# Performance work log

Hardware: AMD Instinct MI355X
Metric: run time of the kernel (lower is better)

The kernel has to match this reference:

```python
import jax, jax.numpy as jnp
import numpy as np

B, L, D, H = 4, 2048, 1024, 16
DH = D // H
EPS = 1e-6

def layer_norm(x, g, b):
    mu = jnp.mean(x, axis=-1, keepdims=True)
    var = jnp.mean(jnp.square(x - mu), axis=-1, keepdims=True)
    return (x - mu) * jax.lax.rsqrt(var + EPS) * g + b

def setup_inputs() -> dict:
    key = jax.random.key(0)
    ks = jax.random.split(key, 8)
    s = 0.02
    return {
        "x": jax.random.normal(ks[0], (B, L, D), jnp.float32),
        "mask": jnp.ones((B, L), jnp.int32),
        "Wq": jax.random.normal(ks[1], (D, D), jnp.float32) * s,
        "bq": jnp.zeros((D,), jnp.float32),
        "Wk": jax.random.normal(ks[2], (D, D), jnp.float32) * s,
        "bk": jnp.zeros((D,), jnp.float32),
        "Wv": jax.random.normal(ks[3], (D, D), jnp.float32) * s,
        "bv": jnp.zeros((D,), jnp.float32),
        "g1": jnp.ones((D,), jnp.float32),
        "b1": jnp.zeros((D,), jnp.float32),
        "g2": jnp.ones((D,), jnp.float32),
        "b2": jnp.zeros((D,), jnp.float32),
        "Wo1": jax.random.normal(ks[4], (D, D), jnp.float32) * s,
        "bo1": jnp.zeros((D,), jnp.float32),
        "Wo2": jax.random.normal(ks[5], (D, D), jnp.float32) * s,
        "bo2": jnp.zeros((D,), jnp.float32),
    }

def reference(x, mask, Wq, bq, Wk, bk, Wv, bv, g1, b1, g2, b2, Wo1, bo1, Wo2, bo2):
    h = layer_norm(x, g1, b1)                                  # [B,L,D]
    q = (h @ Wq + bq).reshape(B, L, H, DH)
    k = (h @ Wk + bk).reshape(B, L, H, DH)
    v = (h @ Wv + bv).reshape(B, L, H, DH)
    scores = jnp.einsum('bqhd,bkhd->bhqk', q, k) / jnp.sqrt(jnp.float32(DH))
    m = mask.astype(scores.dtype)[:, None, None, :]            # [B,1,1,L]
    scores = scores + (1.0 - m) * (-1e30)                      # mask_logits
    probs = jax.nn.softmax(scores, axis=-1)
    attn = jnp.einsum('bhqk,bkhd->bqhd', probs, v).reshape(B, L, D)
    residual = x + attn
    out = layer_norm(residual, g2, b2)
    out = jax.nn.gelu(out @ Wo1 + bo1, approximate=False)      # exact GELU (nn.GELU)
    out = out @ Wo2 + bo2 + residual
    return out
```

## Files before the change

### kernel.cpp

```cpp
#include <hip/hip_runtime.h>
#include <stdint.h>
#include <math.h>

typedef __bf16 bf16_t;
typedef __bf16 bf16x8 __attribute__((ext_vector_type(8)));
typedef __bf16 bf16x4 __attribute__((ext_vector_type(4)));
typedef short short4v __attribute__((ext_vector_type(4)));
typedef float f32x4 __attribute__((ext_vector_type(4)));

#define B_ 4
#define L_ 2048
#define D_ 1024
#define H_ 16
#define DH_ 64
#define M_ (B_ * L_)
#define LOG2E 1.4426950408889634f
#define QSCALE 0.18033688011112042f

__device__ __forceinline__ void gload16(const bf16_t* gsrc, bf16_t* ldst) {
    __builtin_amdgcn_global_load_lds(
        (__attribute__((address_space(1))) void*)(void*)(gsrc),
        (__attribute__((address_space(3))) void*)(ldst), 16, 0, 0);
}

__device__ __forceinline__ float gelu_exact(float v) {
    return 0.5f * v * (1.0f + erff(v * 0.70710678118654752f));
}

__device__ __forceinline__ float fast_exp2(float x) {
#if __has_builtin(__builtin_amdgcn_exp2f)
    return __builtin_amdgcn_exp2f(x);
#else
    return exp2f(x);
#endif
}

__device__ __forceinline__ f32x4 mfma16(bf16x4 a, bf16x4 b, f32x4 c) {
#if __has_builtin(__builtin_amdgcn_mfma_f32_16x16x16_bf16)
    return __builtin_amdgcn_mfma_f32_16x16x16_bf16(a, b, c, 0, 0, 0);
#else
    union U { bf16x4 h; short4v s; };
    U ua, ub; ua.h = a; ub.h = b;
    return __builtin_amdgcn_mfma_f32_16x16x16bf16_1k(ua.s, ub.s, c, 0, 0, 0);
#endif
}

__global__ __launch_bounds__(256) void transpose5(const float* __restrict__ W0, const float* __restrict__ W1,
                                                  const float* __restrict__ W2, const float* __restrict__ W3,
                                                  const float* __restrict__ W4,
                                                  bf16_t* __restrict__ T0, bf16_t* __restrict__ T1,
                                                  bf16_t* __restrict__ T2, bf16_t* __restrict__ T3,
                                                  bf16_t* __restrict__ T4) {
    const float* W; bf16_t* T;
    switch (blockIdx.z) {
        case 0: W = W0; T = T0; break;
        case 1: W = W1; T = T1; break;
        case 2: W = W2; T = T2; break;
        case 3: W = W3; T = T3; break;
        default: W = W4; T = T4; break;
    }
    __shared__ float tile[32][33];
    const int x = threadIdx.x, y0 = threadIdx.y;
    const int bx = blockIdx.x * 32, by = blockIdx.y * 32;
    for (int kk = 0; kk < 4; ++kk)
        tile[y0 + kk * 8][x] = W[(size_t)(by + y0 + kk * 8) * D_ + bx + x];
    __syncthreads();
    for (int kk = 0; kk < 4; ++kk)
        T[(size_t)(bx + y0 + kk * 8) * D_ + by + x] = (bf16_t)tile[x][y0 + kk * 8];
}

__global__ __launch_bounds__(256) void maskbias_kernel(const int* __restrict__ mask,
                                                       float* __restrict__ mb) {
    const int i = blockIdx.x * 256 + threadIdx.x;
    mb[i] = mask[i] ? 0.f : -1.0e30f;
}

__global__ __launch_bounds__(256) void ln1_kernel(const float* __restrict__ x,
                                                  const float* __restrict__ g,
                                                  const float* __restrict__ b,
                                                  bf16_t* __restrict__ h) {
    const int row = blockIdx.x, t = threadIdx.x;
    const float4 v = *(const float4*)(x + (size_t)row * D_ + t * 4);
    float s = v.x + v.y + v.z + v.w;
    float s2 = v.x * v.x + v.y * v.y + v.z * v.z + v.w * v.w;
    for (int m = 1; m < 64; m <<= 1) { s += __shfl_xor(s, m, 64); s2 += __shfl_xor(s2, m, 64); }
    __shared__ float red[2][4];
    if ((t & 63) == 0) { red[0][t >> 6] = s; red[1][t >> 6] = s2; }
    __syncthreads();
    s = red[0][0] + red[0][1] + red[0][2] + red[0][3];
    s2 = red[1][0] + red[1][1] + red[1][2] + red[1][3];
    const float mean = s * (1.f / 1024.f);
    const float var = s2 * (1.f / 1024.f) - mean * mean;
    const float rstd = rsqrtf(var + 1e-6f);
    const float4 gv = *(const float4*)(g + t * 4);
    const float4 bv = *(const float4*)(b + t * 4);
    union { bf16_t h4[4]; uint2 u; } o;
    o.h4[0] = (bf16_t)((v.x - mean) * rstd * gv.x + bv.x);
    o.h4[1] = (bf16_t)((v.y - mean) * rstd * gv.y + bv.y);
    o.h4[2] = (bf16_t)((v.z - mean) * rstd * gv.z + bv.z);
    o.h4[3] = (bf16_t)((v.w - mean) * rstd * gv.w + bv.w);
    *(uint2*)(h + (size_t)row * D_ + t * 4) = o.u;
}

__global__ __launch_bounds__(256) void add_ln2_kernel(const float* __restrict__ x,
                                                      const bf16_t* __restrict__ attnb,
                                                      const float* __restrict__ g,
                                                      const float* __restrict__ b,
                                                      bf16_t* __restrict__ residb,
                                                      bf16_t* __restrict__ h) {
    const int row = blockIdx.x, t = threadIdx.x;
    const float4 xv = *(const float4*)(x + (size_t)row * D_ + t * 4);
    union { uint2 u; bf16_t h4[4]; } ai;
    ai.u = *(const uint2*)(attnb + (size_t)row * D_ + t * 4);
    float4 v;
    v.x = xv.x + (float)ai.h4[0]; v.y = xv.y + (float)ai.h4[1];
    v.z = xv.z + (float)ai.h4[2]; v.w = xv.w + (float)ai.h4[3];
    union { bf16_t h4[4]; uint2 u; } rs;
    rs.h4[0] = (bf16_t)v.x; rs.h4[1] = (bf16_t)v.y; rs.h4[2] = (bf16_t)v.z; rs.h4[3] = (bf16_t)v.w;
    *(uint2*)(residb + (size_t)row * D_ + t * 4) = rs.u;
    float s = v.x + v.y + v.z + v.w;
    float s2 = v.x * v.x + v.y * v.y + v.z * v.z + v.w * v.w;
    for (int m = 1; m < 64; m <<= 1) { s += __shfl_xor(s, m, 64); s2 += __shfl_xor(s2, m, 64); }
    __shared__ float red[2][4];
    if ((t & 63) == 0) { red[0][t >> 6] = s; red[1][t >> 6] = s2; }
    __syncthreads();
    s = red[0][0] + red[0][1] + red[0][2] + red[0][3];
    s2 = red[1][0] + red[1][1] + red[1][2] + red[1][3];
    const float mean = s * (1.f / 1024.f);
    const float var = s2 * (1.f / 1024.f) - mean * mean;
    const float rstd = rsqrtf(var + 1e-6f);
    const float4 gv = *(const float4*)(g + t * 4);
    const float4 bv = *(const float4*)(b + t * 4);
    union { bf16_t h4[4]; uint2 u; } o;
    o.h4[0] = (bf16_t)((v.x - mean) * rstd * gv.x + bv.x);
    o.h4[1] = (bf16_t)((v.y - mean) * rstd * gv.y + bv.y);
    o.h4[2] = (bf16_t)((v.z - mean) * rstd * gv.z + bv.z);
    o.h4[3] = (bf16_t)((v.w - mean) * rstd * gv.w + bv.w);
    *(uint2*)(h + (size_t)row * D_ + t * 4) = o.u;
}

__global__ __launch_bounds__(256) void gemm_qkv(const bf16_t* __restrict__ A,
                                                const bf16_t* __restrict__ BT,
                                                const float* __restrict__ bq,
                                                const float* __restrict__ bk,
                                                const float* __restrict__ bv,
                                                bf16_t* __restrict__ qb,
                                                bf16_t* __restrict__ kb,
                                                bf16_t* __restrict__ vb) {
    constexpr int K = 1024;
    __shared__ bf16_t As[128 * 32];
    __shared__ bf16_t Bs[128 * 32];
    const int t = threadIdx.x;
    const int wave = t >> 6, lane = t & 63;
    const int l16 = lane & 15, g4 = lane >> 4;
    const int bm = blockIdx.x * 128, bn = blockIdx.y * 128;
    const int wm = (wave >> 1) * 64, wn = (wave & 1) * 64;

    f32x4 acc[4][4];
    for (int i = 0; i < 4; ++i)
        for (int j = 0; j < 4; ++j) acc[i][j] = (f32x4){0.f, 0.f, 0.f, 0.f};

    const int ar = t >> 2, ak = (t & 3) * 8;
    const bf16_t* Ag = A + (size_t)(bm + ar) * K + ak;
    const bf16_t* Bg = BT + (size_t)(bn + ar) * K + ak;
    bf16_t* Al = As + t * 8;
    bf16_t* Bl = Bs + t * 8;

    for (int kk = 0; kk < K; kk += 32) {
        __syncthreads();
        gload16(Ag + kk, Al);
        gload16(Ag + (size_t)64 * K + kk, Al + 2048);
        gload16(Bg + kk, Bl);
        gload16(Bg + (size_t)64 * K + kk, Bl + 2048);
        __syncthreads();
        bf16x8 af[4], bfr[4];
        for (int i = 0; i < 4; ++i)
            af[i] = *(const bf16x8*)&As[(wm + i * 16 + l16) * 32 + g4 * 8];
        for (int j = 0; j < 4; ++j)
            bfr[j] = *(const bf16x8*)&Bs[(wn + j * 16 + l16) * 32 + g4 * 8];
        for (int i = 0; i < 4; ++i)
            for (int j = 0; j < 4; ++j)
                acc[i][j] = __builtin_amdgcn_mfma_f32_16x16x32_bf16(af[i], bfr[j], acc[i][j], 0, 0, 0);
    }

    const int which = bn >> 10;
    const int c0 = bn & 1023;
    const float* bias = (which == 0) ? bq : (which == 1) ? bk : bv;
    bf16_t* ob = (which == 0) ? qb : (which == 1) ? kb : vb;
    const float scale = (which == 0) ? QSCALE : 1.0f;

    for (int i = 0; i < 4; ++i)
        for (int j = 0; j < 4; ++j) {
            const int col = c0 + wn + j * 16 + l16;
            const float bvv = bias[col];
            const int row0 = bm + wm + i * 16 + g4 * 4;
            for (int r = 0; r < 4; ++r) {
                const float vv = (acc[i][j][r] + bvv) * scale;
                ob[(size_t)(row0 + r) * D_ + col] = (bf16_t)vv;
            }
        }
}

template <int MODE>
__global__ __launch_bounds__(256) void gemm_bt(const bf16_t* __restrict__ A,
                                               const bf16_t* __restrict__ BT,
                                               const float* __restrict__ bias,
                                               const bf16_t* __restrict__ residb,
                                               bf16_t* __restrict__ outb,
                                               float* __restrict__ outf) {
    constexpr int K = 1024, N = 1024;
    __shared__ bf16_t As[128 * 32];
    __shared__ bf16_t Bs[128 * 32];
    const int t = threadIdx.x;
    const int wave = t >> 6, lane = t & 63;
    const int l16 = lane & 15, g4 = lane >> 4;
    const int bm = blockIdx.x * 128, bn = blockIdx.y * 128;
    const int wm = (wave >> 1) * 64, wn = (wave & 1) * 64;

    f32x4 acc[4][4];
    for (int i = 0; i < 4; ++i)
        for (int j = 0; j < 4; ++j) acc[i][j] = (f32x4){0.f, 0.f, 0.f, 0.f};

    const int ar = t >> 2, ak = (t & 3) * 8;
    const bf16_t* Ag = A + (size_t)(bm + ar) * K + ak;
    const bf16_t* Bg = BT + (size_t)(bn + ar) * K + ak;
    bf16_t* Al = As + t * 8;
    bf16_t* Bl = Bs + t * 8;

    for (int kk = 0; kk < K; kk += 32) {
        __syncthreads();
        gload16(Ag + kk, Al);
        gload16(Ag + (size_t)64 * K + kk, Al + 2048);
        gload16(Bg + kk, Bl);
        gload16(Bg + (size_t)64 * K + kk, Bl + 2048);
        __syncthreads();
        bf16x8 af[4], bfr[4];
        for (int i = 0; i < 4; ++i)
            af[i] = *(const bf16x8*)&As[(wm + i * 16 + l16) * 32 + g4 * 8];
        for (int j = 0; j < 4; ++j)
            bfr[j] = *(const bf16x8*)&Bs[(wn + j * 16 + l16) * 32 + g4 * 8];
        for (int i = 0; i < 4; ++i)
            for (int j = 0; j < 4; ++j)
                acc[i][j] = __builtin_amdgcn_mfma_f32_16x16x32_bf16(af[i], bfr[j], acc[i][j], 0, 0, 0);
    }

    for (int i = 0; i < 4; ++i)
        for (int j = 0; j < 4; ++j) {
            const int col = bn + wn + j * 16 + l16;
            const float bv = bias[col];
            const int row0 = bm + wm + i * 16 + g4 * 4;
            for (int r = 0; r < 4; ++r) {
                float vv = acc[i][j][r] + bv;
                const size_t idx = (size_t)(row0 + r) * N + col;
                if (MODE == 1) {
                    outb[idx] = (bf16_t)gelu_exact(vv);
                } else {
                    outf[idx] = vv + (float)residb[idx];
                }
            }
        }
}

#define KS_STRIDE 72
#define VT_STRIDE 152
__global__ __launch_bounds__(256, 3) void attn_kernel(const bf16_t* __restrict__ q,
                                                      const bf16_t* __restrict__ k,
                                                      const bf16_t* __restrict__ v,
                                                      const float* __restrict__ maskbias,
                                                      bf16_t* __restrict__ attnb) {
    __shared__ char smem[18432 + 19456];
    bf16_t* Ks = (bf16_t*)smem;
    bf16_t* VT = (bf16_t*)(smem + 18432);
    bf16_t* Os = (bf16_t*)smem;

    const int t = threadIdx.x;
    const int wave = t >> 6, lane = t & 63;
    const int l16 = lane & 15, g4 = lane >> 4;
    const int id = blockIdx.x;
    const int xcd = id & 7, seq = id >> 3;
    const int bh = xcd * 8 + (seq >> 4);
    const int b = bh >> 4, h = bh & 15;
    const int q0 = (seq & 15) * 128;

    bf16x8 qf[2][2];
    for (int ti = 0; ti < 2; ++ti)
        for (int c = 0; c < 2; ++c)
            qf[ti][c] = *(const bf16x8*)(q + (size_t)(b * L_ + q0 + wave * 32 + ti * 16 + l16) * D_ +
                                         h * DH_ + c * 32 + g4 * 8);

    f32x4 accO[2][5];
    for (int ti = 0; ti < 2; ++ti)
        for (int dt = 0; dt < 5; ++dt) accO[ti][dt] = (f32x4){0.f, 0.f, 0.f, 0.f};

    const bf16_t one_or_zero = (l16 == 0) ? (bf16_t)1.0f : (bf16_t)0.0f;
    const bf16x4 ones4 = (bf16x4){one_or_zero, one_or_zero, one_or_zero, one_or_zero};

    for (int k0 = 0; k0 < L_; k0 += 128) {
        __syncthreads();
        for (int cc = 0; cc < 4; ++cc) {
            const int c = t + cc * 256;
            const int row = c >> 3, off = (c & 7) * 8;
            *(uint4*)&Ks[row * KS_STRIDE + off] =
                *(const uint4*)(k + (size_t)(b * L_ + k0 + row) * D_ + h * DH_ + off);
        }
        {
            const int d = t & 63, kg = t >> 6;
            for (int k8 = 0; k8 < 4; ++k8) {
                union { uint4 u; bf16_t e[8]; } tv;
                #pragma unroll
                for (int i = 0; i < 8; ++i)
                    tv.e[i] = v[(size_t)(b * L_ + k0 + kg * 32 + k8 * 8 + i) * D_ + h * DH_ + d];
                *(uint4*)&VT[d * VT_STRIDE + kg * 32 + k8 * 8] = tv.u;
            }
        }
        __syncthreads();

        f32x4 s0[8], s1[8];
        #pragma unroll
        for (int tj = 0; tj < 8; ++tj) {
            const bf16x8 kf0 = *(const bf16x8*)&Ks[(tj * 16 + l16) * KS_STRIDE + g4 * 8];
            const bf16x8 kf1 = *(const bf16x8*)&Ks[(tj * 16 + l16) * KS_STRIDE + 32 + g4 * 8];
            f32x4 a = (f32x4){0.f, 0.f, 0.f, 0.f};
            a = __builtin_amdgcn_mfma_f32_16x16x32_bf16(kf0, qf[0][0], a, 0, 0, 0);
            a = __builtin_amdgcn_mfma_f32_16x16x32_bf16(kf1, qf[0][1], a, 0, 0, 0);
            s0[tj] = a;
            f32x4 a2 = (f32x4){0.f, 0.f, 0.f, 0.f};
            a2 = __builtin_amdgcn_mfma_f32_16x16x32_bf16(kf0, qf[1][0], a2, 0, 0, 0);
            a2 = __builtin_amdgcn_mfma_f32_16x16x32_bf16(kf1, qf[1][1], a2, 0, 0, 0);
            s1[tj] = a2;
        }

        bf16x4 pb0[8], pb1[8];
        #pragma unroll
        for (int tj = 0; tj < 8; ++tj) {
            const float4 mb = *(const float4*)&maskbias[b * L_ + k0 + tj * 16 + g4 * 4];
            float p00 = fast_exp2(s0[tj][0] + mb.x), p01 = fast_exp2(s0[tj][1] + mb.y);
            float p02 = fast_exp2(s0[tj][2] + mb.z), p03 = fast_exp2(s0[tj][3] + mb.w);
            float p10 = fast_exp2(s1[tj][0] + mb.x), p11 = fast_exp2(s1[tj][1] + mb.y);
            float p12 = fast_exp2(s1[tj][2] + mb.z), p13 = fast_exp2(s1[tj][3] + mb.w);
            pb0[tj] = (bf16x4){(bf16_t)p00, (bf16_t)p01, (bf16_t)p02, (bf16_t)p03};
            pb1[tj] = (bf16x4){(bf16_t)p10, (bf16_t)p11, (bf16_t)p12, (bf16_t)p13};
        }

        #pragma unroll
        for (int ks = 0; ks < 8; ++ks) {
            #pragma unroll
            for (int dt = 0; dt < 4; ++dt) {
                const bf16x4 va = *(const bf16x4*)&VT[(dt * 16 + l16) * VT_STRIDE + ks * 16 + g4 * 4];
                accO[0][dt] = mfma16(va, pb0[ks], accO[0][dt]);
                accO[1][dt] = mfma16(va, pb1[ks], accO[1][dt]);
            }
            accO[0][4] = mfma16(ones4, pb0[ks], accO[0][4]);
            accO[1][4] = mfma16(ones4, pb1[ks], accO[1][4]);
        }
    }

    __syncthreads();
    for (int ti = 0; ti < 2; ++ti) {
        const float lv = __shfl(accO[ti][4][0], l16, 64);
        const float rl = 1.0f / lv;
        #pragma unroll
        for (int dt = 0; dt < 4; ++dt) {
            bf16x4 o4 = (bf16x4){(bf16_t)(accO[ti][dt][0] * rl), (bf16_t)(accO[ti][dt][1] * rl),
                                 (bf16_t)(accO[ti][dt][2] * rl), (bf16_t)(accO[ti][dt][3] * rl)};
            *(bf16x4*)&Os[(wave * 32 + ti * 16 + l16) * KS_STRIDE + dt * 16 + g4 * 4] = o4;
        }
    }
    __syncthreads();
    for (int cc = 0; cc < 4; ++cc) {
        const int c2 = t + cc * 256;
        const int row = c2 >> 3, k8 = c2 & 7;
        const uint4 vv = *(const uint4*)&Os[row * KS_STRIDE + k8 * 8];
        *(uint4*)&attnb[(size_t)(b * L_ + q0 + row) * D_ + h * DH_ + k8 * 8] = vv;
    }
}

extern "C" void kernel_launch(void* const* d_in, const int* in_sizes, int n_in,
                              void* d_out, int out_size, void* d_ws, size_t ws_size,
                              hipStream_t stream) {
    const float* x    = (const float*)d_in[0];
    const int*   mask = (const int*)d_in[1];
    const float* Wq   = (const float*)d_in[2];
    const float* bq   = (const float*)d_in[3];
    const float* Wk   = (const float*)d_in[4];
    const float* bk   = (const float*)d_in[5];
    const float* Wv   = (const float*)d_in[6];
    const float* bv   = (const float*)d_in[7];
    const float* g1   = (const float*)d_in[8];
    const float* b1   = (const float*)d_in[9];
    const float* g2   = (const float*)d_in[10];
    const float* b2   = (const float*)d_in[11];
    const float* Wo1  = (const float*)d_in[12];
    const float* bo1  = (const float*)d_in[13];
    const float* Wo2  = (const float*)d_in[14];
    const float* bo2  = (const float*)d_in[15];

    char* ws = (char*)d_ws;
    const size_t MBs = 1ull << 20;
    bf16_t* WqkvT = (bf16_t*)(ws + 0 * MBs);
    bf16_t* Wo1T  = (bf16_t*)(ws + 6 * MBs);
    bf16_t* Wo2T  = (bf16_t*)(ws + 8 * MBs);
    bf16_t* h1    = (bf16_t*)(ws + 10 * MBs);
    bf16_t* qb    = (bf16_t*)(ws + 26 * MBs);
    bf16_t* kb    = (bf16_t*)(ws + 42 * MBs);
    bf16_t* vb    = (bf16_t*)(ws + 58 * MBs);
    bf16_t* attnb = (bf16_t*)(ws + 74 * MBs);
    bf16_t* residb= (bf16_t*)(ws + 90 * MBs);
    float*  mbias = (float*)(ws + 106 * MBs);
    bf16_t* h2    = qb;
    bf16_t* gact  = kb;

    transpose5<<<dim3(32, 32, 5), dim3(32, 8), 0, stream>>>(
        Wq, Wk, Wv, Wo1, Wo2,
        WqkvT, WqkvT + (size_t)D_ * D_, WqkvT + (size_t)2 * D_ * D_, Wo1T, Wo2T);

    maskbias_kernel<<<M_ / 256, 256, 0, stream>>>(mask, mbias);

    ln1_kernel<<<M_, 256, 0, stream>>>(x, g1, b1, h1);

    gemm_qkv<<<dim3(M_ / 128, 3 * D_ / 128), 256, 0, stream>>>(h1, WqkvT, bq, bk, bv, qb, kb, vb);

    attn_kernel<<<dim3(1024), 256, 0, stream>>>(qb, kb, vb, mbias, attnb);

    add_ln2_kernel<<<M_, 256, 0, stream>>>(x, attnb, g2, b2, residb, h2);

    const dim3 gg(M_ / 128, D_ / 128);
    gemm_bt<1><<<gg, 256, 0, stream>>>(h2, Wo1T, bo1, nullptr, gact, nullptr);
    gemm_bt<2><<<gg, 256, 0, stream>>>(gact, Wo2T, bo2, residb, nullptr, (float*)d_out);
}
```

Measured before the change: 381.3 us.

## Pre-transpose V once and load K tiles via swizzled direct-to-LDS loads

After: 374.9 us. No clear change (-1.7%).

```diff
diff --git a/kernel.cpp b/kernel.cpp
--- a/kernel.cpp
+++ b/kernel.cpp
@@ -73,6 +73,30 @@
                                                        float* __restrict__ mb) {
     const int i = blockIdx.x * 256 + threadIdx.x;
     mb[i] = mask[i] ? 0.f : -1.0e30f;
+}
+
+#define VTR_STRIDE 76
+__global__ __launch_bounds__(256) void vtrans_kernel(const bf16_t* __restrict__ vb,
+                                                     bf16_t* __restrict__ vt) {
+    __shared__ bf16_t tile[128 * VTR_STRIDE];
+    const int t = threadIdx.x;
+    const int bh = blockIdx.y, b = bh >> 4, h = bh & 15;
+    const int k0 = blockIdx.x * 128;
+    #pragma unroll
+    for (int it = 0; it < 4; ++it) {
+        const int row = it * 32 + (t >> 3), c8 = (t & 7) * 8;
+        *(uint4*)&tile[row * VTR_STRIDE + c8] =
+            *(const uint4*)(vb + (size_t)(b * L_ + k0 + row) * D_ + h * DH_ + c8);
+    }
+    __syncthreads();
+    #pragma unroll
+    for (int it = 0; it < 4; ++it) {
+        const int d = it * 16 + (t >> 4), kg = (t & 15) * 8;
+        union { uint4 u; bf16_t e[8]; } tv;
+        #pragma unroll
+        for (int j = 0; j < 8; ++j) tv.e[j] = tile[(kg + j) * VTR_STRIDE + d];
+        *(uint4*)&vt[((size_t)bh * DH_ + d) * L_ + k0 + kg] = tv.u;
+    }
 }
 
 __global__ __launch_bounds__(256) void ln1_kernel(const float* __restrict__ x,
@@ -261,17 +285,16 @@
         }
 }
 
-#define KS_STRIDE 72
 #define VT_STRIDE 152
+#define OS_STRIDE 72
 __global__ __launch_bounds__(256, 3) void attn_kernel(const bf16_t* __restrict__ q,
                                                       const bf16_t* __restrict__ k,
-                                                      const bf16_t* __restrict__ v,
+                                                      const bf16_t* __restrict__ vt,
                                                       const float* __restrict__ maskbias,
                                                       bf16_t* __restrict__ attnb) {
-    __shared__ char smem[18432 + 19456];
-    bf16_t* Ks = (bf16_t*)smem;
-    bf16_t* VT = (bf16_t*)(smem + 18432);
-    bf16_t* Os = (bf16_t*)smem;
+    __shared__ bf16_t Ks[128 * 64];
+    __shared__ bf16_t VT[64 * VT_STRIDE];
+    bf16_t* Os = VT;
 
     const int t = threadIdx.x;
     const int wave = t >> 6, lane = t & 63;
@@ -295,31 +318,35 @@
     const bf16_t one_or_zero = (l16 == 0) ? (bf16_t)1.0f : (bf16_t)0.0f;
     const bf16x4 ones4 = (bf16x4){one_or_zero, one_or_zero, one_or_zero, one_or_zero};
 
+    const int krow0 = t >> 3, kcg = t & 7;
+    const int klcg = kcg ^ (krow0 & 7);
+    const bf16_t* kbase = k + (size_t)(b * L_ + krow0) * D_ + h * DH_ + klcg * 8;
+    bf16_t* kdst = Ks + t * 8;
+    const int vrow0 = t >> 4, vkg = t & 15;
+    const bf16_t* vbase = vt + ((size_t)bh * DH_ + vrow0) * L_ + vkg * 8;
+    bf16_t* vdst = &VT[vrow0 * VT_STRIDE + vkg * 8];
+
+    const int kb0 = l16 * 64 + ((g4 ^ (l16 & 7)) * 8);
+    const int kb1 = l16 * 64 + (((g4 + 4) ^ (l16 & 7)) * 8);
+    const int vrb = l16 * VT_STRIDE + g4 * 4;
+
     for (int k0 = 0; k0 < L_; k0 += 128) {
         __syncthreads();
-        for (int cc = 0; cc < 4; ++cc) {
-            const int c = t + cc * 256;
-            const int row = c >> 3, off = (c & 7) * 8;
-            *(uint4*)&Ks[row * KS_STRIDE + off] =
-                *(const uint4*)(k + (size_t)(b * L_ + k0 + row) * D_ + h * DH_ + off);
-        }
-        {
-            const int d = t & 63, kg = t >> 6;
-            for (int k8 = 0; k8 < 4; ++k8) {
-                union { uint4 u; bf16_t e[8]; } tv;
-                #pragma unroll
-                for (int i = 0; i < 8; ++i)
-                    tv.e[i] = v[(size_t)(b * L_ + k0 + kg * 32 + k8 * 8 + i) * D_ + h * DH_ + d];
-                *(uint4*)&VT[d * VT_STRIDE + kg * 32 + k8 * 8] = tv.u;
-            }
+        #pragma unroll
+        for (int it = 0; it < 4; ++it)
+            gload16(kbase + (size_t)(k0 + it * 32) * D_, kdst + it * 2048);
+        #pragma unroll
+        for (int it = 0; it < 4; ++it) {
+            const uint4 vv = *(const uint4*)(vbase + (size_t)(it * 16) * L_ + k0);
+            *(uint4*)(vdst + it * 16 * VT_STRIDE) = vv;
         }
         __syncthreads();
 
         f32x4 s0[8], s1[8];
         #pragma unroll
         for (int tj = 0; tj < 8; ++tj) {
-            const bf16x8 kf0 = *(const bf16x8*)&Ks[(tj * 16 + l16) * KS_STRIDE + g4 * 8];
-            const bf16x8 kf1 = *(const bf16x8*)&Ks[(tj * 16 + l16) * KS_STRIDE + 32 + g4 * 8];
+            const bf16x8 kf0 = *(const bf16x8*)&Ks[tj * 1024 + kb0];
+            const bf16x8 kf1 = *(const bf16x8*)&Ks[tj * 1024 + kb1];
             f32x4 a = (f32x4){0.f, 0.f, 0.f, 0.f};
             a = __builtin_amdgcn_mfma_f32_16x16x32_bf16(kf0, qf[0][0], a, 0, 0, 0);
             a = __builtin_amdgcn_mfma_f32_16x16x32_bf16(kf1, qf[0][1], a, 0, 0, 0);
@@ -346,7 +373,7 @@
         for (int ks = 0; ks < 8; ++ks) {
             #pragma unroll
             for (int dt = 0; dt < 4; ++dt) {
-                const bf16x4 va = *(const bf16x4*)&VT[(dt * 16 + l16) * VT_STRIDE + ks * 16 + g4 * 4];
+                const bf16x4 va = *(const bf16x4*)&VT[vrb + dt * 16 * VT_STRIDE + ks * 16];
                 accO[0][dt] = mfma16(va, pb0[ks], accO[0][dt]);
                 accO[1][dt] = mfma16(va, pb1[ks], accO[1][dt]);
             }
@@ -363,14 +390,14 @@
         for (int dt = 0; dt < 4; ++dt) {
             bf16x4 o4 = (bf16x4){(bf16_t)(accO[ti][dt][0] * rl), (bf16_t)(accO[ti][dt][1] * rl),
                                  (bf16_t)(accO[ti][dt][2] * rl), (bf16_t)(accO[ti][dt][3] * rl)};
-            *(bf16x4*)&Os[(wave * 32 + ti * 16 + l16) * KS_STRIDE + dt * 16 + g4 * 4] = o4;
+            *(bf16x4*)&Os[(wave * 32 + ti * 16 + l16) * OS_STRIDE + dt * 16 + g4 * 4] = o4;
         }
     }
     __syncthreads();
     for (int cc = 0; cc < 4; ++cc) {
         const int c2 = t + cc * 256;
         const int row = c2 >> 3, k8 = c2 & 7;
-        const uint4 vv = *(const uint4*)&Os[row * KS_STRIDE + k8 * 8];
+        const uint4 vv = *(const uint4*)&Os[row * OS_STRIDE + k8 * 8];
         *(uint4*)&attnb[(size_t)(b * L_ + q0 + row) * D_ + h * DH_ + k8 * 8] = vv;
     }
 }
@@ -401,6 +428,7 @@
     bf16_t* Wo1T  = (bf16_t*)(ws + 6 * MBs);
     bf16_t* Wo2T  = (bf16_t*)(ws + 8 * MBs);
     bf16_t* h1    = (bf16_t*)(ws + 10 * MBs);
+    bf16_t* vtb   = h1;
     bf16_t* qb    = (bf16_t*)(ws + 26 * MBs);
     bf16_t* kb    = (bf16_t*)(ws + 42 * MBs);
     bf16_t* vb    = (bf16_t*)(ws + 58 * MBs);
@@ -420,7 +448,9 @@
 
     gemm_qkv<<<dim3(M_ / 128, 3 * D_ / 128), 256, 0, stream>>>(h1, WqkvT, bq, bk, bv, qb, kb, vb);
 
-    attn_kernel<<<dim3(1024), 256, 0, stream>>>(qb, kb, vb, mbias, attnb);
+    vtrans_kernel<<<dim3(L_ / 128, B_ * H_), 256, 0, stream>>>(vb, vtb);
+
+    attn_kernel<<<dim3(1024), 256, 0, stream>>>(qb, kb, vtb, mbias, attnb);
 
     add_ln2_kernel<<<M_, 256, 0, stream>>>(x, attnb, g2, b2, residb, h2);
 
```
